# Performance work log

Hardware: AMD Instinct MI355X
Metric: run time of the kernel (lower is better)

## Reference

```python
import jax, jax.numpy as jnp
import numpy as np

N = 100000   # nodes
E = 800000   # directed edges (before self loops)
D = 300      # feature dim (SGConv(300, 300))


def setup_inputs() -> dict:
    key = jax.random.key(0)
    k1, k2, k3, k4 = jax.random.split(key, 4)
    x = jax.random.normal(k1, (N, D), dtype=jnp.float32)
    edge_index = jax.random.randint(k2, (2, E), 0, N, dtype=jnp.int32)
    # Linear(300, 300) params (kaiming-uniform-ish scale)
    bound = 1.0 / np.sqrt(D)
    W = jax.random.uniform(k3, (D, D), jnp.float32, -bound, bound)
    b = jax.random.uniform(k4, (D,), jnp.float32, -bound, bound)
    return {"x": x, "edge_index": edge_index, "W": W, "b": b}


def _sgc_forward(x, edge_index, W, b):
    n = x.shape[0]
    # --- GCN normalization with self loops (PyG SGConv defaults, K=1) ---
    loop = jnp.arange(n, dtype=edge_index.dtype)
    row = jnp.concatenate([edge_index[0], loop])   # source nodes
    col = jnp.concatenate([edge_index[1], loop])   # target nodes (aggregation index)
    deg = jax.ops.segment_sum(jnp.ones_like(col, dtype=x.dtype), col, num_segments=n)
    dinv = jnp.where(deg > 0, jax.lax.rsqrt(deg), 0.0)
    w = dinv[row] * dinv[col]                      # [E+N] edge norm
    # --- one hop of sparse propagation: out[c] += w * x[r] ---
    h = jax.ops.segment_sum(x[row] * w[:, None], col, num_segments=n)  # [N, D]
    # --- linear map ---
    h = h @ W.T + b
    # --- relu (dropout p=0 is identity) ---
    h = jax.nn.relu(h)
    # --- F.normalize: row-wise L2 with eps clamp ---
    norm = jnp.linalg.norm(h, axis=-1, keepdims=True)
    return h / jnp.maximum(norm, 1e-12)


def reference(x, edge_index, W, b):
    return _sgc_forward(x, edge_index, W, b)
```

## Files before the change

kernel.cpp:

```cpp
#include <hip/hip_runtime.h>
#include <hip/hip_bf16.h>
#include <stdint.h>

#define D 300
#define KP 320
#define JP 304
#define NT 19

typedef __hip_bfloat16 bf16;
typedef __bf16 bf16x8 __attribute__((ext_vector_type(8)));
typedef unsigned short us8 __attribute__((ext_vector_type(8)));
typedef float f32x4 __attribute__((ext_vector_type(4)));

static __device__ __forceinline__ unsigned short f2bu(float f) {
    bf16 h = __float2bfloat16(f);
    return *reinterpret_cast<unsigned short*>(&h);
}
static __device__ __forceinline__ float bulo(unsigned int u) {
    return __uint_as_float(u << 16);
}
static __device__ __forceinline__ float buhi(unsigned int u) {
    return __uint_as_float(u & 0xffff0000u);
}
static __device__ __forceinline__ void gload_lds16(const void* g, void* l) {
    __builtin_amdgcn_global_load_lds(
        (const __attribute__((address_space(1))) unsigned int*)g,
        (__attribute__((address_space(3))) unsigned int*)l, 16, 0, 0);
}

__global__ void k_count(const int* __restrict__ col, int* __restrict__ deg, int e) {
    int i = blockIdx.x * 256 + threadIdx.x;
    if (i < e) atomicAdd(&deg[col[i]], 1);
}

__global__ void k_scanA(const int* __restrict__ deg, int* __restrict__ ex,
                        float* __restrict__ dinv, int* __restrict__ bsum, int n) {
    __shared__ int sh[256];
    int tid = threadIdx.x;
    int base = blockIdx.x * 1024 + tid * 4;
    int v[4]; int s = 0;
#pragma unroll
    for (int t = 0; t < 4; t++) {
        int i = base + t;
        v[t] = (i < n) ? deg[i] : 0;
        if (i < n) dinv[i] = rsqrtf((float)(v[t] + 1));
        s += v[t];
    }
    sh[tid] = s;
    __syncthreads();
    for (int off = 1; off < 256; off <<= 1) {
        int t = (tid >= off) ? sh[tid - off] : 0;
        __syncthreads();
        sh[tid] += t;
        __syncthreads();
    }
    int excl = sh[tid] - s;
#pragma unroll
    for (int t = 0; t < 4; t++) {
        int i = base + t;
        if (i < n) ex[i] = excl;
        excl += v[t];
    }
    if (tid == 255) bsum[blockIdx.x] = sh[255];
}

__global__ void k_scanB(const int* __restrict__ bsum, int* __restrict__ bexc, int nb) {
    __shared__ int sh[256];
    int tid = threadIdx.x;
    int s = (tid < nb) ? bsum[tid] : 0;
    sh[tid] = s;
    __syncthreads();
    for (int off = 1; off < 256; off <<= 1) {
        int t = (tid >= off) ? sh[tid - off] : 0;
        __syncthreads();
        sh[tid] += t;
        __syncthreads();
    }
    bexc[tid] = sh[tid] - s;
}

__global__ void k_scanC(int* __restrict__ starts, const int* __restrict__ bexc, int n) {
    int i = blockIdx.x * 256 + threadIdx.x;
    if (i < n) starts[i] += bexc[i >> 10];
}

__global__ void k_fill(const int* __restrict__ ei, const float* __restrict__ dinv,
                       const int* __restrict__ starts, int* __restrict__ cursor,
                       uint2* __restrict__ edges, int e) {
    int i = blockIdx.x * 256 + threadIdx.x;
    if (i < e) {
        int r = ei[i];
        int c = ei[e + i];
        int p = atomicAdd(&cursor[c], 1);
        edges[starts[c] + p] = make_uint2((unsigned int)r,
                                          __float_as_uint(dinv[r] * dinv[c]));
    }
}

__global__ void k_twb(const float* __restrict__ W, unsigned short* __restrict__ wbp) {
    int idx = blockIdx.x * 256 + threadIdx.x;
    if (idx < JP * KP) {
        int i = idx & 7;
        int lrow = (idx >> 3) & 15;
        int kg = (idx >> 7) & 3;
        int q = idx >> 9;
        int kk = q / 19, t = q - kk * 19;
        int j = t * 16 + lrow;
        int k = kk * 32 + kg * 8 + i;
        wbp[idx] = (j < D && k < D) ? f2bu(W[j * D + k]) : (unsigned short)0;
    }
}

__global__ __launch_bounds__(256)
void k_zmm(const float* __restrict__ x, const unsigned short* __restrict__ wbp,
           unsigned short* __restrict__ zb, int n) {
    __shared__ unsigned short Wsh[2][JP * 32];
    int tid = threadIdx.x;
    int lane = tid & 63, wid = tid >> 6;
    int r0 = blockIdx.x * 64 + wid * 16;
    int lrow = lane & 15, kg = lane >> 4;

    int soff[5];
#pragma unroll
    for (int j = 0; j < 5; j++) {
        int i = wid + 4 * j;
        soff[j] = (i < 19) ? (i * 1024 + lane * 16) : -1;
    }
    const char* wb = (const char*)wbp;

    int arow = r0 + lrow; if (arow >= n) arow = n - 1;
    const float* xr = x + (size_t)arow * D;

    f32x4 acc[NT];
#pragma unroll
    for (int t = 0; t < NT; t++) acc[t] = f32x4{0.f, 0.f, 0.f, 0.f};

    float4 pa, pb;
    {
        int c = kg * 8;
        pa = *(const float4*)(xr + c);
        pb = *(const float4*)(xr + c + 4);
#pragma unroll
        for (int j = 0; j < 5; j++)
            if (soff[j] >= 0) gload_lds16(wb + soff[j], (char*)&Wsh[0][0] + soff[j]);
    }
    __syncthreads();

    for (int kk = 0; kk < KP / 32; kk++) {
        float4 na, nb2;
        if (kk < KP / 32 - 1) {
            int c = (kk + 1) * 32 + kg * 8;
            int clo = (c <= 296) ? c : 0;
            int chi = (c <= 292) ? c + 4 : 0;
            na  = *(const float4*)(xr + clo);
            nb2 = *(const float4*)(xr + chi);
            int gof = (kk + 1) * (JP * 64);
            char* lbase = (char*)&Wsh[(kk + 1) & 1][0];
#pragma unroll
            for (int j = 0; j < 5; j++)
                if (soff[j] >= 0) gload_lds16(wb + gof + soff[j], lbase + soff[j]);
        }
        us8 au;
        au[0] = f2bu(pa.x); au[1] = f2bu(pa.y); au[2] = f2bu(pa.z); au[3] = f2bu(pa.w);
        au[4] = f2bu(pb.x); au[5] = f2bu(pb.y); au[6] = f2bu(pb.z); au[7] = f2bu(pb.w);
        bf16x8 av = __builtin_bit_cast(bf16x8, au);
        const unsigned short* bbase = &Wsh[kk & 1][0] + lane * 8;
#pragma unroll
        for (int t = 0; t < NT; t++) {
            bf16x8 bv = __builtin_bit_cast(bf16x8, *(const us8*)(bbase + t * 512));
            acc[t] = __builtin_amdgcn_mfma_f32_16x16x32_bf16(av, bv, acc[t], 0, 0, 0);
        }
        __syncthreads();
        pa = na; pb = nb2;
    }

#pragma unroll
    for (int r = 0; r < 4; r++) {
        int g0 = r0 + kg * 4 + r;
        if (g0 < n) {
            unsigned short* zp0 = zb + (size_t)g0 * JP;
#pragma unroll
            for (int t = 0; t < NT; t++) {
                int j = t * 16 + lrow;
                zp0[j] = f2bu(acc[t][r]);
            }
        }
    }
}

__global__ void k_zgather(const uint2* __restrict__ zb2, const uint2* __restrict__ edges,
                          const int* __restrict__ starts, const int* __restrict__ deg,
                          const float* __restrict__ dinv, const float* __restrict__ bias,
                          float* __restrict__ out, int n) {
    int w = (blockIdx.x * blockDim.x + threadIdx.x) >> 6;
    if (w >= n) return;
    int lane = threadIdx.x & 63;
    int s = starts[w];
    int cnt = deg[w];
    float dc = dinv[w];
    const bool p2 = lane < 12;
    float a0 = 0.f, a1 = 0.f, a2 = 0.f, a3 = 0.f;
    float a4 = 0.f, a5 = 0.f, a6 = 0.f, a7 = 0.f;
    const uint2 Z = make_uint2(0u, 0u);

#define GACC(ua, ub, wgt)                                                     \
    {                                                                         \
        a0 += (wgt) * bulo((ua).x); a1 += (wgt) * buhi((ua).x);               \
        a2 += (wgt) * bulo((ua).y); a3 += (wgt) * buhi((ua).y);               \
        a4 += (wgt) * bulo((ub).x); a5 += (wgt) * buhi((ub).x);               \
        a6 += (wgt) * bulo((ub).y); a7 += (wgt) * buhi((ub).y);               \
    }

    int t = 0;
    for (; t + 4 <= cnt; t += 4) {
        uint2 e0 = edges[s + t],     e1 = edges[s + t + 1];
        uint2 e2 = edges[s + t + 2], e3 = edges[s + t + 3];
        const uint2* q0 = zb2 + (size_t)e0.x * 76 + lane;
        const uint2* q1 = zb2 + (size_t)e1.x * 76 + lane;
        const uint2* q2 = zb2 + (size_t)e2.x * 76 + lane;
        const uint2* q3 = zb2 + (size_t)e3.x * 76 + lane;
        uint2 u0a = q0[0], u1a = q1[0], u2a = q2[0], u3a = q3[0];
        uint2 u0b = p2 ? q0[64] : Z;
        uint2 u1b = p2 ? q1[64] : Z;
        uint2 u2b = p2 ? q2[64] : Z;
        uint2 u3b = p2 ? q3[64] : Z;
        float w0 = __uint_as_float(e0.y), w1 = __uint_as_float(e1.y);
        float w2 = __uint_as_float(e2.y), w3 = __uint_as_float(e3.y);
        GACC(u0a, u0b, w0);
        GACC(u1a, u1b, w1);
        GACC(u2a, u2b, w2);
        GACC(u3a, u3b, w3);
    }
    for (; t < cnt; t++) {
        uint2 ed = edges[s + t];
        float wg = __uint_as_float(ed.y);
        const uint2* q = zb2 + (size_t)ed.x * 76 + lane;
        uint2 ua = q[0];
        uint2 ub = p2 ? q[64] : Z;
        GACC(ua, ub, wg);
    }
    {
        float sw = dc * dc;
        const uint2* q = zb2 + (size_t)w * 76 + lane;
        uint2 ua = q[0];
        uint2 ub = p2 ? q[64] : Z;
        GACC(ua, ub, sw);
    }
#undef GACC

    float4 b0 = *(const float4*)(bias + 4 * lane);
    float4 b1 = {0.f, 0.f, 0.f, 0.f};
    const bool wr2 = lane < 11;
    if (wr2) b1 = *(const float4*)(bias + 256 + 4 * lane);
    float v0 = fmaxf(a0 + b0.x, 0.f), v1 = fmaxf(a1 + b0.y, 0.f);
    float v2 = fmaxf(a2 + b0.z, 0.f), v3 = fmaxf(a3 + b0.w, 0.f);
    float v4 = fmaxf(a4 + b1.x, 0.f), v5 = fmaxf(a5 + b1.y, 0.f);
    float v6 = fmaxf(a6 + b1.z, 0.f), v7 = fmaxf(a7 + b1.w, 0.f);
    float sq = v0 * v0 + v1 * v1 + v2 * v2 + v3 * v3
             + v4 * v4 + v5 * v5 + v6 * v6 + v7 * v7;
    sq += __shfl_xor(sq, 1);
    sq += __shfl_xor(sq, 2);
    sq += __shfl_xor(sq, 4);
    sq += __shfl_xor(sq, 8);
    sq += __shfl_xor(sq, 16);
    sq += __shfl_xor(sq, 32);
    float sc = rsqrtf(fmaxf(sq, 1e-24f));

    float* op = out + (size_t)w * D;
    f32x4 o0 = {v0 * sc, v1 * sc, v2 * sc, v3 * sc};
    __builtin_nontemporal_store(o0, (f32x4*)(op + 4 * lane));
    if (wr2) {
        f32x4 o1 = {v4 * sc, v5 * sc, v6 * sc, v7 * sc};
        __builtin_nontemporal_store(o1, (f32x4*)(op + 256 + 4 * lane));
    }
}

extern "C" void kernel_launch(void* const* d_in, const int* in_sizes, int n_in,
                              void* d_out, int out_size, void* d_ws, size_t ws_size,
                              hipStream_t stream) {
    const float* x  = (const float*)d_in[0];
    const int*   ei = (const int*)d_in[1];
    const float* W  = (const float*)d_in[2];
    const float* b  = (const float*)d_in[3];
    float* out = (float*)d_out;
    int n = in_sizes[0] / D;
    int e = in_sizes[1] / 2;

    char* p = (char*)d_ws;
    unsigned short* zb = (unsigned short*)p; p += (size_t)n * JP * 2;
    int* deg = (int*)p;         p += (size_t)n * 4;
    int* cursor = (int*)p;      p += (size_t)n * 4;
    float* dinv = (float*)p;    p += (size_t)n * 4;
    int* starts = (int*)p;      p += (size_t)n * 4;
    p = (char*)(((uintptr_t)p + 15) & ~(uintptr_t)15);
    uint2* edges = (uint2*)p;   p += (size_t)e * 8;
    int* bsum = (int*)p;        p += 256 * 4;
    int* bexc = (int*)p;        p += 256 * 4;
    p = (char*)(((uintptr_t)p + 15) & ~(uintptr_t)15);
    unsigned short* wbp = (unsigned short*)p; p += (size_t)JP * KP * 2;

    int nb = (n + 1023) / 1024;

    (void)hipMemsetAsync(deg, 0, (size_t)n * 8, stream);
    k_count<<<(e + 255) / 256, 256, 0, stream>>>(ei + e, deg, e);
    k_scanA<<<nb, 256, 0, stream>>>(deg, starts, dinv, bsum, n);
    k_scanB<<<1, 256, 0, stream>>>(bsum, bexc, nb);
    k_scanC<<<(n + 255) / 256, 256, 0, stream>>>(starts, bexc, n);
    k_fill <<<(e + 255) / 256, 256, 0, stream>>>(ei, dinv, starts, cursor, edges, e);
    k_twb  <<<(JP * KP + 255) / 256, 256, 0, stream>>>(W, wbp);
    k_zmm  <<<(n + 63) / 64, 256, 0, stream>>>(x, wbp, zb, n);
    k_zgather<<<(n + 3) / 4, 256, 0, stream>>>((const uint2*)zb, edges, starts, deg,
                                               dinv, b, out, n);
}
```

Measured before the change: 238.1 us.

## Merge preprocessing kernels into fewer launches and drop the scan-add pass

The degree count and the weight bf16 packing now share one launch, using block-index ranges. The CSR edge fill runs as extra blocks inside the dense x·W matmul kernel, so the two independent stages overlap. The separate scanC pass is removed; each consumer now adds the block offset (ex[c] + bexc[c>>10]) on the fly. This cuts three kernel launches and their serialization gaps, at the cost of mixing atomic-heavy fill blocks with matmul blocks and adding an extra indexed load per lookup.

```diff
diff --git a/kernel.cpp b/kernel.cpp
--- a/kernel.cpp
+++ b/kernel.cpp
@@ -28,9 +28,26 @@
         (__attribute__((address_space(3))) unsigned int*)l, 16, 0, 0);
 }
 
-__global__ void k_count(const int* __restrict__ col, int* __restrict__ deg, int e) {
-    int i = blockIdx.x * 256 + threadIdx.x;
-    if (i < e) atomicAdd(&deg[col[i]], 1);
+__global__ void k_count_twb(const int* __restrict__ col, int* __restrict__ deg, int e,
+                            const float* __restrict__ W, unsigned short* __restrict__ wbp,
+                            int cb) {
+    int bid = blockIdx.x;
+    if (bid < cb) {
+        int i = bid * 256 + threadIdx.x;
+        if (i < e) atomicAdd(&deg[col[i]], 1);
+    } else {
+        int idx = (bid - cb) * 256 + threadIdx.x;
+        if (idx < JP * KP) {
+            int i = idx & 7;
+            int lrow = (idx >> 3) & 15;
+            int kg = (idx >> 7) & 3;
+            int q = idx >> 9;
+            int kk = q / 19, t = q - kk * 19;
+            int j = t * 16 + lrow;
+            int k = kk * 32 + kg * 8 + i;
+            wbp[idx] = (j < D && k < D) ? f2bu(W[j * D + k]) : (unsigned short)0;
+        }
+    }
 }
 
 __global__ void k_scanA(const int* __restrict__ deg, int* __restrict__ ex,
@@ -79,42 +96,24 @@
     bexc[tid] = sh[tid] - s;
 }
 
-__global__ void k_scanC(int* __restrict__ starts, const int* __restrict__ bexc, int n) {
-    int i = blockIdx.x * 256 + threadIdx.x;
-    if (i < n) starts[i] += bexc[i >> 10];
-}
-
-__global__ void k_fill(const int* __restrict__ ei, const float* __restrict__ dinv,
-                       const int* __restrict__ starts, int* __restrict__ cursor,
-                       uint2* __restrict__ edges, int e) {
-    int i = blockIdx.x * 256 + threadIdx.x;
-    if (i < e) {
-        int r = ei[i];
-        int c = ei[e + i];
-        int p = atomicAdd(&cursor[c], 1);
-        edges[starts[c] + p] = make_uint2((unsigned int)r,
-                                          __float_as_uint(dinv[r] * dinv[c]));
-    }
-}
-
-__global__ void k_twb(const float* __restrict__ W, unsigned short* __restrict__ wbp) {
-    int idx = blockIdx.x * 256 + threadIdx.x;
-    if (idx < JP * KP) {
-        int i = idx & 7;
-        int lrow = (idx >> 3) & 15;
-        int kg = (idx >> 7) & 3;
-        int q = idx >> 9;
-        int kk = q / 19, t = q - kk * 19;
-        int j = t * 16 + lrow;
-        int k = kk * 32 + kg * 8 + i;
-        wbp[idx] = (j < D && k < D) ? f2bu(W[j * D + k]) : (unsigned short)0;
-    }
-}
-
 __global__ __launch_bounds__(256)
-void k_zmm(const float* __restrict__ x, const unsigned short* __restrict__ wbp,
-           unsigned short* __restrict__ zb, int n) {
+void k_zmm_fill(const float* __restrict__ x, const unsigned short* __restrict__ wbp,
+                unsigned short* __restrict__ zb, int n, int zblocks,
+                const int* __restrict__ ei, const float* __restrict__ dinv,
+                const int* __restrict__ ex, const int* __restrict__ bexc,
+                int* __restrict__ cursor, uint2* __restrict__ edges, int e) {
     __shared__ unsigned short Wsh[2][JP * 32];
+    if (blockIdx.x >= zblocks) {
+        int i = (int)(blockIdx.x - zblocks) * 256 + threadIdx.x;
+        if (i < e) {
+            int r = ei[i];
+            int c = ei[e + i];
+            int p = atomicAdd(&cursor[c], 1);
+            edges[ex[c] + bexc[c >> 10] + p] =
+                make_uint2((unsigned int)r, __float_as_uint(dinv[r] * dinv[c]));
+        }
+        return;
+    }
     int tid = threadIdx.x;
     int lane = tid & 63, wid = tid >> 6;
     int r0 = blockIdx.x * 64 + wid * 16;
@@ -189,13 +188,13 @@
 }
 
 __global__ void k_zgather(const uint2* __restrict__ zb2, const uint2* __restrict__ edges,
-                          const int* __restrict__ starts, const int* __restrict__ deg,
-                          const float* __restrict__ dinv, const float* __restrict__ bias,
-                          float* __restrict__ out, int n) {
+                          const int* __restrict__ ex, const int* __restrict__ bexc,
+                          const int* __restrict__ deg, const float* __restrict__ dinv,
+                          const float* __restrict__ bias, float* __restrict__ out, int n) {
     int w = (blockIdx.x * blockDim.x + threadIdx.x) >> 6;
     if (w >= n) return;
     int lane = threadIdx.x & 63;
-    int s = starts[w];
+    int s = ex[w] + bexc[w >> 10];
     int cnt = deg[w];
     float dc = dinv[w];
     const bool p2 = lane < 12;
@@ -291,7 +290,7 @@
     int* deg = (int*)p;         p += (size_t)n * 4;
     int* cursor = (int*)p;      p += (size_t)n * 4;
     float* dinv = (float*)p;    p += (size_t)n * 4;
-    int* starts = (int*)p;      p += (size_t)n * 4;
+    int* ex = (int*)p;          p += (size_t)n * 4;
     p = (char*)(((uintptr_t)p + 15) & ~(uintptr_t)15);
     uint2* edges = (uint2*)p;   p += (size_t)e * 8;
     int* bsum = (int*)p;        p += 256 * 4;
@@ -300,15 +299,17 @@
     unsigned short* wbp = (unsigned short*)p; p += (size_t)JP * KP * 2;
 
     int nb = (n + 1023) / 1024;
+    int cb = (e + 255) / 256;
+    int tb = (JP * KP + 255) / 256;
+    int zblocks = (n + 63) / 64;
+    int fb = (e + 255) / 256;
 
     (void)hipMemsetAsync(deg, 0, (size_t)n * 8, stream);
-    k_count<<<(e + 255) / 256, 256, 0, stream>>>(ei + e, deg, e);
-    k_scanA<<<nb, 256, 0, stream>>>(deg, starts, dinv, bsum, n);
+    k_count_twb<<<cb + tb, 256, 0, stream>>>(ei + e, deg, e, W, wbp, cb);
+    k_scanA<<<nb, 256, 0, stream>>>(deg, ex, dinv, bsum, n);
     k_scanB<<<1, 256, 0, stream>>>(bsum, bexc, nb);
-    k_scanC<<<(n + 255) / 256, 256, 0, stream>>>(starts, bexc, n);
-    k_fill <<<(e + 255) / 256, 256, 0, stream>>>(ei, dinv, starts, cursor, edges, e);
-    k_twb  <<<(JP * KP + 255) / 256, 256, 0, stream>>>(W, wbp);
-    k_zmm  <<<(n + 63) / 64, 256, 0, stream>>>(x, wbp, zb, n);
-    k_zgather<<<(n + 3) / 4, 256, 0, stream>>>((const uint2*)zb, edges, starts, deg,
-                                               dinv, b, out, n);
-}
+    k_zmm_fill<<<zblocks + fb, 256, 0, stream>>>(x, wbp, zb, n, zblocks,
+                                                 ei, dinv, ex, bexc, cursor, edges, e);
+    k_zgather<<<(n + 3) / 4, 256, 0, stream>>>((const uint2*)zb, edges, ex, bexc,
+                                               deg, dinv, b, out, n);
+}
```

Measured after the change: 222.9 us. -6.4%, faster.
